# Optimization experiments

Measured on AMD Instinct MI355X. Metric: run time of the kernel, lower is better.

Reference implementation:

```python
import jax, jax.numpy as jnp
import numpy as np

N_NODES = 50000
N_EDGES = 800000
D_FEAT = 128
UNITS = 256
K = 3


def setup_inputs() -> dict:
    key = jax.random.key(0)
    k1, k2, k3, k4 = jax.random.split(key, 4)
    x = jax.random.normal(k1, (N_NODES, D_FEAT), dtype=jnp.float32)
    edge_index = jax.random.randint(k2, (2, N_EDGES), 0, N_NODES, dtype=jnp.int32)
    edge_weight = jnp.ones((N_EDGES,), dtype=jnp.float32)
    # glorot-uniform kernel [(K+1)*D, UNITS], zero bias
    fan_in, fan_out = D_FEAT * (K + 1), UNITS
    limit = np.sqrt(6.0 / (fan_in + fan_out)).astype(np.float32)
    kernel = jax.random.uniform(k3, (fan_in, fan_out), minval=-limit, maxval=limit, dtype=jnp.float32)
    bias = jnp.zeros((UNITS,), dtype=jnp.float32)
    return {"x": x, "edge_index": edge_index, "edge_weight": edge_weight,
            "kernel": kernel, "bias": bias}


def reference(x, edge_index, edge_weight, kernel, bias):
    n = x.shape[0]
    row, col = edge_index[0], edge_index[1]
    # symmetric GCN normalization (renorm=False: normalize first, then self-loops w=1)
    deg = jax.ops.segment_sum(edge_weight, row, num_segments=n)
    deg_inv_sqrt = jnp.where(deg > 0, jax.lax.rsqrt(jnp.where(deg > 0, deg, 1.0)), 0.0)
    normed_w = deg_inv_sqrt[row] * edge_weight * deg_inv_sqrt[col]
    loop = jnp.arange(n, dtype=row.dtype)
    row2 = jnp.concatenate([row, loop])
    col2 = jnp.concatenate([col, loop])
    w2 = jnp.concatenate([normed_w, jnp.ones((n,), dtype=normed_w.dtype)])
    # K-hop propagation, collecting each hop
    xs = [x]
    h = x
    for _ in range(K):
        msg = h[col2] * w2[:, None]            # [E+N, D] gather + scale
        h = jax.ops.segment_sum(msg, row2, num_segments=n)  # scatter-sum
        xs.append(h)
    hcat = jnp.concatenate(xs, axis=-1)        # [N, (K+1)*D]
    out = hcat @ kernel + bias
    return jax.nn.relu(out)
```

## Files before the change

kernel.cpp:

```cpp
#include <hip/hip_runtime.h>

#define NN 50000
#define NP 50048
#define NE 800000
#define D 128
#define UNITS 256
#define KTOT 512
#define SCAN_NB 196
#define NREP 16
#define CONV_NB 6250
#define COUNT_NB 3125

typedef __attribute__((ext_vector_type(8))) short short8;
typedef __attribute__((ext_vector_type(4))) float floatx4;

__device__ inline unsigned short f2b(float f) {
    unsigned u = __float_as_uint(f);
    return (unsigned short)((u + 0x7fff + ((u >> 16) & 1)) >> 16);
}
__device__ inline float2 bx2f(unsigned v) {
    float2 r;
    r.x = __uint_as_float(v << 16);
    r.y = __uint_as_float(v & 0xffff0000u);
    return r;
}

__global__ __launch_bounds__(256) void count_prep_kernel(const int* __restrict__ row,
                                                         int* __restrict__ cnt16,
                                                         int* __restrict__ rank,
                                                         const float* __restrict__ x,
                                                         unsigned* __restrict__ xb,
                                                         const float* __restrict__ W,
                                                         short* __restrict__ Wt) {
    __shared__ float tile[32][33];
    int b = blockIdx.x;
    if (b < COUNT_NB) {
        int e = b * 256 + threadIdx.x;
        if (e < NE) {
            int r = row[e];
            int rep = (e >> 6) & (NREP - 1);
            rank[e] = atomicAdd(&cnt16[rep * NN + r], 1);
        }
    } else if (b < COUNT_NB + CONV_NB) {
        int t = (b - COUNT_NB) * 256 + threadIdx.x;
        float4 v = ((const float4*)x)[t];
        uint2 o;
        o.x = (unsigned)f2b(v.x) | ((unsigned)f2b(v.y) << 16);
        o.y = (unsigned)f2b(v.z) | ((unsigned)f2b(v.w) << 16);
        ((uint2*)xb)[t] = o;
    } else if (b < COUNT_NB + CONV_NB + 128) {
        int bb = b - COUNT_NB - CONV_NB;
        int kb = (bb & 15) * 32;
        int nb = (bb >> 4) * 32;
        int tx = threadIdx.x & 31, ty = threadIdx.x >> 5;
        for (int i = 0; i < 32; i += 8)
            tile[ty + i][tx] = W[(size_t)(kb + ty + i) * UNITS + nb + tx];
        __syncthreads();
        for (int i = 0; i < 32; i += 8)
            Wt[(size_t)(nb + ty + i) * KTOT + kb + tx] = (short)f2b(tile[tx][ty + i]);
    } else {
        uint4 z = {0u, 0u, 0u, 0u};
        uint4* x4 = (uint4*)xb;
        for (int i = threadIdx.x; i < 4 * 48 * 16; i += 256) {
            int chunk = i / (48 * 16);
            int rem = i - chunk * (48 * 16);
            int rowp = NN + (rem >> 4);
            x4[((size_t)chunk * NP + rowp) * 16 + (rem & 15)] = z;
        }
    }
}

__global__ __launch_bounds__(256) void scanA_kernel(int* __restrict__ cnt16,
                                                    int* __restrict__ row_ptr,
                                                    int* __restrict__ bsum) {
    __shared__ int s[256];
    int t = threadIdx.x;
    int idx = blockIdx.x * 256 + t;
    int tot = 0;
    if (idx < NN) {
        int c[NREP];
#pragma unroll
        for (int r = 0; r < NREP; ++r) c[r] = cnt16[r * NN + idx];
        int run = 0;
#pragma unroll
        for (int r = 0; r < NREP; ++r) {
            cnt16[r * NN + idx] = run;
            run += c[r];
        }
        tot = run;
    }
    s[t] = tot;
    __syncthreads();
    for (int off = 1; off < 256; off <<= 1) {
        int add = (t >= off) ? s[t - off] : 0;
        __syncthreads();
        s[t] += add;
        __syncthreads();
    }
    if (idx < NN) row_ptr[idx] = s[t] - tot;
    if (t == 255) bsum[blockIdx.x] = s[255];
}

__global__ __launch_bounds__(256) void scanC_kernel(int* __restrict__ row_ptr,
                                                    const int* __restrict__ bsum) {
    __shared__ int soff_s;
    int b = blockIdx.x, t = threadIdx.x;
    if (t < 64) {
        int acc = 0;
        for (int i = t; i < b; i += 64) acc += bsum[i];
#pragma unroll
        for (int off = 32; off; off >>= 1) acc += __shfl_down(acc, off);
        if (t == 0) soff_s = acc;
    }
    __syncthreads();
    int idx = b * 256 + t;
    if (idx < NN) row_ptr[idx] += soff_s;
    if (b == 0 && t == 0) row_ptr[NN] = NE;
}

__global__ void fill_kernel(const int* __restrict__ row, const int* __restrict__ col,
                            const float* __restrict__ w, const int* __restrict__ rank,
                            const int* __restrict__ row_ptr, const int* __restrict__ cnt16,
                            int2* __restrict__ edges, int E) {
    int e = blockIdx.x * blockDim.x + threadIdx.x;
    if (e >= E) return;
    int r = row[e];
    int rep = (e >> 6) & (NREP - 1);
    int pos = row_ptr[r] + cnt16[rep * NN + r] + rank[e];
    edges[pos] = make_int2(col[e], __float_as_int(w[e]));
}

__global__ __launch_bounds__(256) void degdis_kernel(const int* __restrict__ row_ptr,
                                                     const int2* __restrict__ edges,
                                                     float* __restrict__ dis) {
    int node = blockIdx.x * 4 + (threadIdx.x >> 6);
    int l = threadIdx.x & 63;
    if (node >= NN) return;
    int beg = row_ptr[node], end = row_ptr[node + 1];
    float s = 0.f;
    for (int e = beg + l; e < end; e += 64) s += __int_as_float(edges[e].y);
#pragma unroll
    for (int off = 32; off; off >>= 1) s += __shfl_down(s, off);
    if (l == 0) dis[node] = s > 0.f ? rsqrtf(s) : 0.f;
}

__device__ inline void acc8(float* acc, uint4 v, float w) {
    float2 f0 = bx2f(v.x), f1 = bx2f(v.y), f2 = bx2f(v.z), f3 = bx2f(v.w);
    acc[0] = fmaf(w, f0.x, acc[0]); acc[1] = fmaf(w, f0.y, acc[1]);
    acc[2] = fmaf(w, f1.x, acc[2]); acc[3] = fmaf(w, f1.y, acc[3]);
    acc[4] = fmaf(w, f2.x, acc[4]); acc[5] = fmaf(w, f2.y, acc[5]);
    acc[6] = fmaf(w, f3.x, acc[6]); acc[7] = fmaf(w, f3.y, acc[7]);
}

template <bool NORM>
__global__ __launch_bounds__(256) void gather_kernel(const unsigned* __restrict__ hprev,
                                                     unsigned* __restrict__ hnext,
                                                     const int* __restrict__ row_ptr,
                                                     int2* __restrict__ edges,
                                                     const float* __restrict__ dis) {
    int node = blockIdx.x * 4 + (threadIdx.x >> 6);
    if (node >= NN) return;
    int l = threadIdx.x & 63;
    int g = l >> 4;
    int s = l & 15;
    const uint4* hp4 = (const uint4*)hprev;
    int beg = row_ptr[node], end = row_ptr[node + 1];
    float dr = NORM ? dis[node] : 1.f;
    int last = (end - 1 > beg) ? end - 1 : beg;
    if (last >= NE) last = NE - 1;

    float acc[8] = {0.f, 0.f, 0.f, 0.f, 0.f, 0.f, 0.f, 0.f};
    int2 M[4];
#pragma unroll
    for (int b = 0; b < 4; ++b) {
        int i = beg + b * 4 + g;
        M[b] = edges[i < end ? i : last];
    }
    for (int e = beg; e < end; e += 16) {
        int2 E[4];
#pragma unroll
        for (int b = 0; b < 4; ++b) E[b] = M[b];
        int en = e + 16;
        if (en < end) {
#pragma unroll
            for (int b = 0; b < 4; ++b) {
                int j = en + b * 4 + g;
                M[b] = edges[j < end ? j : last];
            }
        }
        float wgt[4];
        uint4 v[4];
#pragma unroll
        for (int b = 0; b < 4; ++b) {
            float wv = __int_as_float(E[b].y);
            if (NORM) wv *= dr * dis[E[b].x];
            int i = e + b * 4 + g;
            wgt[b] = (i < end) ? wv : 0.f;
            v[b] = hp4[(size_t)E[b].x * 16 + s];
        }
#pragma unroll
        for (int b = 0; b < 4; ++b) acc8(acc, v[b], wgt[b]);
        if (NORM && s == 0) {
#pragma unroll
            for (int b = 0; b < 4; ++b) {
                int i = e + b * 4 + g;
                if (i < end) edges[i].y = __float_as_int(wgt[b]);
            }
        }
    }
#pragma unroll
    for (int i = 0; i < 8; ++i) {
        acc[i] += __shfl_xor(acc[i], 16);
        acc[i] += __shfl_xor(acc[i], 32);
    }
    if (g == 0) {
        uint4 sv = hp4[(size_t)node * 16 + s];
        acc8(acc, sv, 1.f);
        uint4 o;
        o.x = (unsigned)f2b(acc[0]) | ((unsigned)f2b(acc[1]) << 16);
        o.y = (unsigned)f2b(acc[2]) | ((unsigned)f2b(acc[3]) << 16);
        o.z = (unsigned)f2b(acc[4]) | ((unsigned)f2b(acc[5]) << 16);
        o.w = (unsigned)f2b(acc[6]) | ((unsigned)f2b(acc[7]) << 16);
        ((uint4*)hnext)[(size_t)node * 16 + s] = o;
    }
}

#define BK 32
#define NIT (KTOT / BK)
#define GLDS(g, l)                                                                      \
    __builtin_amdgcn_global_load_lds((const __attribute__((address_space(1))) void*)(g), \
                                     (__attribute__((address_space(3))) void*)(l), 16, 0, 0)

__global__ __launch_bounds__(256, 2) void gemm_mfma(const short* __restrict__ A0,
                                                    const short* __restrict__ Wt,
                                                    const float* __restrict__ bias,
                                                    float* __restrict__ C) {
    __shared__ short As[2][128 * BK];
    __shared__ short Bs[2][128 * BK];
    const int nwg = 782;
    int orig = blockIdx.x;
    int xcd = orig & 7;
    int q = nwg >> 3, r = nwg & 7;
    int wgid = (xcd < r ? xcd * (q + 1) : r * (q + 1) + (xcd - r) * q) + (orig >> 3);
    const int m0 = (wgid >> 1) * 128;
    const int n0 = (wgid & 1) * 128;

    const int t = threadIdx.x;
    const int w = t >> 6;
    const int l = t & 63;
    const int wr = (w >> 1) * 64;
    const int wc = (w & 1) * 64;
    const int lm = l & 15;
    const int lg = l >> 4;
    const int srow = l >> 2;
    const int sc = ((l & 3) ^ ((l >> 3) & 3)) * 8;

    floatx4 zero = {0.f, 0.f, 0.f, 0.f};
    floatx4 acc[4][4];
#pragma unroll
    for (int rr = 0; rr < 4; ++rr)
#pragma unroll
        for (int cc = 0; cc < 4; ++cc) acc[rr][cc] = zero;

#define STAGE(IT, BUF)                                                                  \
    do {                                                                                \
        int kk = (IT) * BK;                                                             \
        const short* Asrc = A0 + (size_t)(kk >> 7) * ((size_t)NP * 128) + (kk & 127);   \
        const short* Bsrc = Wt + kk;                                                    \
        GLDS(Asrc + (size_t)(m0 + w * 32 + srow) * D + sc, &As[BUF][(w * 32) * 32 + l * 8]); \
        GLDS(Asrc + (size_t)(m0 + w * 32 + 16 + srow) * D + sc,                         \
             &As[BUF][(w * 32 + 16) * 32 + l * 8]);                                     \
        GLDS(Bsrc + (size_t)(n0 + w * 32 + srow) * KTOT + sc,                           \
             &Bs[BUF][(w * 32) * 32 + l * 8]);                                          \
        GLDS(Bsrc + (size_t)(n0 + w * 32 + 16 + srow) * KTOT + sc,                      \
             &Bs[BUF][(w * 32 + 16) * 32 + l * 8]);                                     \
    } while (0)

    STAGE(0, 0);
    for (int it = 0; it < NIT; ++it) {
        int cur = it & 1;
        if (it + 1 < NIT) {
            STAGE(it + 1, cur ^ 1);
            asm volatile("s_waitcnt vmcnt(4)" ::: "memory");
        } else {
            asm volatile("s_waitcnt vmcnt(0)" ::: "memory");
        }
        __builtin_amdgcn_s_barrier();
        __builtin_amdgcn_sched_barrier(0);
        short8 af[4], bf[4];
#pragma unroll
        for (int rr = 0; rr < 4; ++rr) {
            int rowv = wr + rr * 16 + lm;
            int p = lg ^ ((rowv >> 1) & 3);
            af[rr] = *(const short8*)&As[cur][rowv * BK + p * 8];
        }
#pragma unroll
        for (int cc = 0; cc < 4; ++cc) {
            int rowv = wc + cc * 16 + lm;
            int p = lg ^ ((rowv >> 1) & 3);
            bf[cc] = *(const short8*)&Bs[cur][rowv * BK + p * 8];
        }
#pragma unroll
        for (int rr = 0; rr < 4; ++rr)
#pragma unroll
            for (int cc = 0; cc < 4; ++cc)
                acc[rr][cc] = __builtin_amdgcn_mfma_f32_16x16x32_bf16(af[rr], bf[cc],
                                                                      acc[rr][cc], 0, 0, 0);
        __builtin_amdgcn_sched_barrier(0);
        __builtin_amdgcn_s_barrier();
    }
#undef STAGE

    const int q4 = lg * 4;
#pragma unroll
    for (int rr = 0; rr < 4; ++rr) {
#pragma unroll
        for (int i = 0; i < 4; ++i) {
            int m = m0 + wr + rr * 16 + q4 + i;
            if (m < NN) {
#pragma unroll
                for (int cc = 0; cc < 4; ++cc) {
                    int n = n0 + wc + cc * 16 + lm;
                    float v = acc[rr][cc][i] + bias[n];
                    C[(size_t)m * UNITS + n] = fmaxf(v, 0.f);
                }
            }
        }
    }
}

extern "C" void kernel_launch(void* const* d_in, const int* in_sizes, int n_in,
                              void* d_out, int out_size, void* d_ws, size_t ws_size,
                              hipStream_t stream) {
    const float* x = (const float*)d_in[0];
    const int* ei = (const int*)d_in[1];
    const float* ew_in = (const float*)d_in[2];
    const float* W = (const float*)d_in[3];
    const float* bias = (const float*)d_in[4];
    float* out = (float*)d_out;

    const int* row = ei;
    const int* col = ei + NE;

    float* dis = (float*)d_ws;
    int* cnt16 = (int*)(dis + NN);
    int* rank = cnt16 + NREP * NN;
    int* bsum = rank + NE;
    int* row_ptr = bsum + 256;
    int2* edges = (int2*)(row_ptr + NN + 2);
    unsigned* xb = (unsigned*)(((uintptr_t)(edges + NE) + 15) & ~(uintptr_t)15);
    unsigned* h1b = xb + (size_t)NP * 64;
    unsigned* h2b = h1b + (size_t)NP * 64;
    unsigned* h3b = h2b + (size_t)NP * 64;
    short* Wt = (short*)(h3b + (size_t)NP * 64);

    hipMemsetAsync(cnt16, 0, NREP * NN * sizeof(int), stream);

    count_prep_kernel<<<COUNT_NB + CONV_NB + 128 + 1, 256, 0, stream>>>(row, cnt16, rank,
                                                                        x, xb, W, Wt);
    scanA_kernel<<<SCAN_NB, 256, 0, stream>>>(cnt16, row_ptr, bsum);
    scanC_kernel<<<SCAN_NB, 256, 0, stream>>>(row_ptr, bsum);
    fill_kernel<<<(NE + 255) / 256, 256, 0, stream>>>(row, col, ew_in, rank, row_ptr, cnt16,
                                                      edges, NE);
    degdis_kernel<<<(NN + 3) / 4, 256, 0, stream>>>(row_ptr, edges, dis);

    int gat_blocks = (NN + 3) / 4;
    gather_kernel<true><<<gat_blocks, 256, 0, stream>>>(xb, h1b, row_ptr, edges, dis);
    gather_kernel<false><<<gat_blocks, 256, 0, stream>>>(h1b, h2b, row_ptr, edges, dis);
    gather_kernel<false><<<gat_blocks, 256, 0, stream>>>(h2b, h3b, row_ptr, edges, dis);

    gemm_mfma<<<782, 256, 0, stream>>>((const short*)xb, Wt, bias, out);
}
```

Before: 300.0 us.

## Split gather feature dim across two blocks and precompute normalized edge weights

Moves edge weight normalization out of the first gather into a separate normw kernel, so all three gather passes share one simple unified kernel. Each node's 128-feature row is now split into two halves handled by different blocks, with 8 edge groups per wave instead of 4. The block index is swizzled so paired halves run close together. This doubles the number of blocks and the edge-list reads in exchange for more parallelism and a shorter per-wave dependency chain, and adds one extra kernel launch.

After: 352.0 us. 1.17x slower.

```diff
diff --git a/kernel.cpp b/kernel.cpp
--- a/kernel.cpp
+++ b/kernel.cpp
@@ -144,6 +144,20 @@
     if (l == 0) dis[node] = s > 0.f ? rsqrtf(s) : 0.f;
 }
 
+__global__ __launch_bounds__(256) void normw_kernel(const int* __restrict__ row_ptr,
+                                                    int2* __restrict__ edges,
+                                                    const float* __restrict__ dis) {
+    int node = blockIdx.x * 4 + (threadIdx.x >> 6);
+    int l = threadIdx.x & 63;
+    if (node >= NN) return;
+    int beg = row_ptr[node], end = row_ptr[node + 1];
+    float dr = dis[node];
+    for (int e = beg + l; e < end; e += 64) {
+        int2 ed = edges[e];
+        edges[e].y = __float_as_int(__int_as_float(ed.y) * dr * dis[ed.x]);
+    }
+}
+
 __device__ inline void acc8(float* acc, uint4 v, float w) {
     float2 f0 = bx2f(v.x), f1 = bx2f(v.y), f2 = bx2f(v.z), f3 = bx2f(v.w);
     acc[0] = fmaf(w, f0.x, acc[0]); acc[1] = fmaf(w, f0.y, acc[1]);
@@ -152,76 +166,68 @@
     acc[6] = fmaf(w, f3.x, acc[6]); acc[7] = fmaf(w, f3.y, acc[7]);
 }
 
-template <bool NORM>
 __global__ __launch_bounds__(256) void gather_kernel(const unsigned* __restrict__ hprev,
                                                      unsigned* __restrict__ hnext,
                                                      const int* __restrict__ row_ptr,
-                                                     int2* __restrict__ edges,
-                                                     const float* __restrict__ dis) {
-    int node = blockIdx.x * 4 + (threadIdx.x >> 6);
+                                                     const int2* __restrict__ edges) {
+    int b = blockIdx.x;
+    int half = (b >> 2) & 1;
+    int rest = ((b >> 3) << 2) | (b & 3);
+    int node = rest * 4 + (threadIdx.x >> 6);
     if (node >= NN) return;
     int l = threadIdx.x & 63;
-    int g = l >> 4;
-    int s = l & 15;
+    int g = l >> 3;
+    int s = l & 7;
+    int fb = half * 8 + s;
     const uint4* hp4 = (const uint4*)hprev;
     int beg = row_ptr[node], end = row_ptr[node + 1];
-    float dr = NORM ? dis[node] : 1.f;
     int last = (end - 1 > beg) ? end - 1 : beg;
     if (last >= NE) last = NE - 1;
 
     float acc[8] = {0.f, 0.f, 0.f, 0.f, 0.f, 0.f, 0.f, 0.f};
-    int2 M[4];
-#pragma unroll
-    for (int b = 0; b < 4; ++b) {
-        int i = beg + b * 4 + g;
-        M[b] = edges[i < end ? i : last];
+    int2 M[2];
+#pragma unroll
+    for (int bb = 0; bb < 2; ++bb) {
+        int i = beg + bb * 8 + g;
+        M[bb] = edges[i < end ? i : last];
     }
     for (int e = beg; e < end; e += 16) {
-        int2 E[4];
-#pragma unroll
-        for (int b = 0; b < 4; ++b) E[b] = M[b];
+        int2 E[2];
+        E[0] = M[0]; E[1] = M[1];
         int en = e + 16;
         if (en < end) {
 #pragma unroll
-            for (int b = 0; b < 4; ++b) {
-                int j = en + b * 4 + g;
-                M[b] = edges[j < end ? j : last];
+            for (int bb = 0; bb < 2; ++bb) {
+                int j = en + bb * 8 + g;
+                M[bb] = edges[j < end ? j : last];
             }
         }
-        float wgt[4];
-        uint4 v[4];
-#pragma unroll
-        for (int b = 0; b < 4; ++b) {
-            float wv = __int_as_float(E[b].y);
-            if (NORM) wv *= dr * dis[E[b].x];
-            int i = e + b * 4 + g;
-            wgt[b] = (i < end) ? wv : 0.f;
-            v[b] = hp4[(size_t)E[b].x * 16 + s];
-        }
-#pragma unroll
-        for (int b = 0; b < 4; ++b) acc8(acc, v[b], wgt[b]);
-        if (NORM && s == 0) {
-#pragma unroll
-            for (int b = 0; b < 4; ++b) {
-                int i = e + b * 4 + g;
-                if (i < end) edges[i].y = __float_as_int(wgt[b]);
-            }
-        }
+        float wgt[2];
+        uint4 v[2];
+#pragma unroll
+        for (int bb = 0; bb < 2; ++bb) {
+            int i = e + bb * 8 + g;
+            wgt[bb] = (i < end) ? __int_as_float(E[bb].y) : 0.f;
+            v[bb] = hp4[(size_t)E[bb].x * 16 + fb];
+        }
+        acc8(acc, v[0], wgt[0]);
+        acc8(acc, v[1], wgt[1]);
     }
 #pragma unroll
     for (int i = 0; i < 8; ++i) {
+        acc[i] += __shfl_xor(acc[i], 8);
         acc[i] += __shfl_xor(acc[i], 16);
         acc[i] += __shfl_xor(acc[i], 32);
     }
     if (g == 0) {
-        uint4 sv = hp4[(size_t)node * 16 + s];
+        uint4 sv = hp4[(size_t)node * 16 + fb];
         acc8(acc, sv, 1.f);
         uint4 o;
         o.x = (unsigned)f2b(acc[0]) | ((unsigned)f2b(acc[1]) << 16);
         o.y = (unsigned)f2b(acc[2]) | ((unsigned)f2b(acc[3]) << 16);
         o.z = (unsigned)f2b(acc[4]) | ((unsigned)f2b(acc[5]) << 16);
         o.w = (unsigned)f2b(acc[6]) | ((unsigned)f2b(acc[7]) << 16);
-        ((uint4*)hnext)[(size_t)node * 16 + s] = o;
+        ((uint4*)hnext)[(size_t)node * 16 + fb] = o;
     }
 }
 
@@ -363,11 +369,12 @@
     fill_kernel<<<(NE + 255) / 256, 256, 0, stream>>>(row, col, ew_in, rank, row_ptr, cnt16,
                                                       edges, NE);
     degdis_kernel<<<(NN + 3) / 4, 256, 0, stream>>>(row_ptr, edges, dis);
-
-    int gat_blocks = (NN + 3) / 4;
-    gather_kernel<true><<<gat_blocks, 256, 0, stream>>>(xb, h1b, row_ptr, edges, dis);
-    gather_kernel<false><<<gat_blocks, 256, 0, stream>>>(h1b, h2b, row_ptr, edges, dis);
-    gather_kernel<false><<<gat_blocks, 256, 0, stream>>>(h2b, h3b, row_ptr, edges, dis);
+    normw_kernel<<<(NN + 3) / 4, 256, 0, stream>>>(row_ptr, edges, dis);
+
+    int gat_blocks = 2 * ((NN + 3) / 4);
+    gather_kernel<<<gat_blocks, 256, 0, stream>>>(xb, h1b, row_ptr, edges);
+    gather_kernel<<<gat_blocks, 256, 0, stream>>>(h1b, h2b, row_ptr, edges);
+    gather_kernel<<<gat_blocks, 256, 0, stream>>>(h2b, h3b, row_ptr, edges);
 
     gemm_mfma<<<782, 256, 0, stream>>>((const short*)xb, Wt, bias, out);
 }
```
